# Kernel tuning notes

Hardware: AMD Instinct MI355X
Metric: run time of the kernel (lower is better)

Reference implementation:

```python
import jax, jax.numpy as jnp
import numpy as np
from jax import lax

# Static problem configuration (SAModule(ratio=0.25, r=0.2, MLP([35,64,64,128])))
B, N, C_IN = 8, 4096, 32
RATIO, R, K = 0.25, 0.2, 64   # K == max_num_neighbors
M = int(N * RATIO)            # centroids per cloud after FPS
NEG = -1e10


def setup_inputs() -> dict:
    key = jax.random.key(0)
    ks = jax.random.split(key, 6)
    x = jax.random.normal(ks[0], (B * N, C_IN), jnp.float32)
    pos = jax.random.uniform(ks[1], (B * N, 3), jnp.float32)  # unit cube -> r=0.2 balls are non-trivial
    batch = jnp.repeat(jnp.arange(B, dtype=jnp.int32), N)
    def lin(k, fan_in, fan_out):
        return jax.random.normal(k, (fan_in, fan_out), jnp.float32) * (1.0 / np.sqrt(fan_in))
    W1 = lin(ks[2], C_IN + 3, 64); b1 = jnp.zeros((64,), jnp.float32)
    W2 = lin(ks[3], 64, 64);       b2 = jnp.zeros((64,), jnp.float32)
    W3 = lin(ks[4], 64, 128);      b3 = jnp.zeros((128,), jnp.float32)
    return {"x": x, "pos": pos, "batch": batch,
            "W1": W1, "b1": b1, "W2": W2, "b2": b2, "W3": W3, "b3": b3}


def _fps_one(p):
    """Farthest-point sampling on one cloud p:[N,3] -> idx:[M] (deterministic start at 0)."""
    def body(carry, _):
        dmin, last = carry
        d = jnp.sum((p - p[last]) ** 2, axis=-1)         # [N] sq-dist to last picked point
        dmin = jnp.minimum(dmin, d)
        nxt = jnp.argmax(dmin).astype(jnp.int32)
        return (dmin, nxt), nxt
    init = (jnp.full((N,), 1e10, jnp.float32), jnp.int32(0))
    _, rest = lax.scan(body, init, None, length=M - 1)
    return jnp.concatenate([jnp.zeros((1,), jnp.int32), rest])


def _sa_one(p, xb, ib, W1, b1, W2, b2, W3, b3):
    """Radius ball-query + PointNetConv (gather -> MLP -> masked scatter-max) on one cloud."""
    ctr = p[ib]                                              # [M,3] sampled centroids
    d2 = jnp.sum((ctr[:, None, :] - p[None, :, :]) ** 2, -1)  # [M,N]
    negd, nbr = lax.top_k(-d2, K)                            # K nearest per centroid
    valid = (-negd) <= R * R                                 # inside-ball mask [M,K]
    xj = xb[nbr]                                             # [M,K,C_IN] gathered features
    rel = p[nbr] - ctr[:, None, :]                           # [M,K,3] relative positions
    h = jnp.concatenate([xj, rel], axis=-1)                  # message input [x_j, pos_j - pos_i]
    h = jax.nn.relu(h @ W1 + b1)
    h = jax.nn.relu(h @ W2 + b2)
    h = h @ W3 + b3                                          # plain last layer (PyG MLP plain_last)
    h = jnp.where(valid[..., None], h, NEG)
    return jnp.max(h, axis=1)                                # max aggregation -> [M,128]


def reference(x, pos, batch, W1, b1, W2, b2, W3, b3):
    pos3 = pos.reshape(B, N, 3)
    x3 = x.reshape(B, N, C_IN)
    idx = jax.vmap(_fps_one)(pos3)                           # [B,M]
    conv = lambda p, xb, ib: _sa_one(p, xb, ib, W1, b1, W2, b2, W3, b3)
    x_out = jax.vmap(conv)(pos3, x3, idx)                    # [B,M,128]
    pos_out = jnp.take_along_axis(pos3, idx[..., None], axis=1)  # [B,M,3]
    batch_out = jnp.repeat(jnp.arange(B, dtype=batch.dtype), M)
    return x_out.reshape(B * M, -1), pos_out.reshape(B * M, 3), batch_out
```

## Files before the change

### kernel.cpp

```cpp
#include <hip/hip_runtime.h>
#include <hip/hip_bf16.h>

#define BB 8
#define NN 4096
#define CIN 32
#define MM 1024
#define KNB 64
#define CAND 1024
#define FPS_T 256
#define FPS_PPT 16
#define ROWS 72

typedef __attribute__((ext_vector_type(8))) short  short8;
typedef __attribute__((ext_vector_type(4))) float  f32x4;

__device__ __forceinline__ float sq3(float dx, float dy, float dz) {
    return __fadd_rn(__fadd_rn(__fmul_rn(dx, dx), __fmul_rn(dy, dy)), __fmul_rn(dz, dz));
}

__device__ __forceinline__ unsigned short f2bf(float v) {
    union { __hip_bfloat16 b; unsigned short u; } cv;
    cv.b = __float2bfloat16(v);
    return cv.u;
}
__device__ __forceinline__ float bf2f(unsigned short u) {
    union { unsigned short u; __hip_bfloat16 b; } cv;
    cv.u = u;
    return __bfloat162float(cv.b);
}

static __device__ __forceinline__ f32x4 mfma16(short8 a, short8 b, f32x4 c) {
    return __builtin_amdgcn_mfma_f32_16x16x32_bf16(a, b, c, 0, 0, 0);
}

template<int CTRL>
__device__ __forceinline__ unsigned long long dpp_maxkey(unsigned long long k) {
    unsigned int lo = (unsigned int)k;
    unsigned int hi = (unsigned int)(k >> 32);
    unsigned int nlo = (unsigned int)__builtin_amdgcn_update_dpp((int)lo, (int)lo, CTRL, 0xF, 0xF, false);
    unsigned int nhi = (unsigned int)__builtin_amdgcn_update_dpp((int)hi, (int)hi, CTRL, 0xF, 0xF, false);
    unsigned long long nk = ((unsigned long long)nhi << 32) | (unsigned long long)nlo;
    return nk > k ? nk : k;
}

__global__ __launch_bounds__(256) void prep_kernel(
    const float* __restrict__ W1, const float* __restrict__ W2,
    const float* __restrict__ W3, unsigned short* __restrict__ wf)
{
    int gid = blockIdx.x * 256 + threadIdx.x;
    const float* W; int K, Ncol, base, slot;
    if (gid < 1024)      { W = W1; K = 35; Ncol = 64;  base = 0;     slot = gid; }
    else if (gid < 2048) { W = W2; K = 64; Ncol = 64;  base = 8192;  slot = gid - 1024; }
    else                 { W = W3; K = 64; Ncol = 128; base = 16384; slot = gid - 2048; }
    int lane = slot & 63, h = (slot >> 6) & 1, kstep = (slot >> 7) & 1, tile = slot >> 8;
    int col = tile * 16 + (lane & 15), quad = lane >> 4;
#pragma unroll
    for (int j = 0; j < 8; ++j) {
        int k = kstep * 32 + quad * 8 + j;
        float wv = (k < K) ? W[k * Ncol + col] : 0.0f;
        unsigned short hi = f2bf(wv);
        unsigned short v = h ? f2bf(wv - bf2f(hi)) : hi;
        wf[base + slot * 8 + j] = v;
    }
}

__global__ __launch_bounds__(FPS_T) void fps_kernel(
    const float* __restrict__ pos, int* __restrict__ idx_ws, float* __restrict__ out)
{
    const int b = blockIdx.x;
    const int t = threadIdx.x;
    __shared__ float4 plds4[NN];
    __shared__ int    chosen[MM];
    __shared__ __align__(16) unsigned long long part[2][FPS_T / 64];

    const float* P = pos + (size_t)b * NN * 3;
    for (int i = t; i < NN; i += FPS_T) {
        float4 v;
        v.x = P[3 * i]; v.y = P[3 * i + 1]; v.z = P[3 * i + 2]; v.w = 0.0f;
        plds4[i] = v;
    }
    if (t == 0) chosen[0] = 0;
    __syncthreads();

    float px[FPS_PPT], py[FPS_PPT], pz[FPS_PPT], dmin[FPS_PPT];
#pragma unroll
    for (int s = 0; s < FPS_PPT; ++s) {
        int i = t + FPS_T * s;
        float4 v = plds4[i];
        px[s] = v.x; py[s] = v.y; pz[s] = v.z;
        dmin[s] = 1e10f;
    }

    int win = 0;
    for (int it = 1; it < MM; ++it) {
        float4 wc = plds4[win];
        const float lx = wc.x, ly = wc.y, lz = wc.z;
        float bv = -1.0f;
        int   bi = 0;
#pragma unroll
        for (int s = 0; s < FPS_PPT; ++s) {
            float dx = px[s] - lx, dy = py[s] - ly, dz = pz[s] - lz;
            float d  = sq3(dx, dy, dz);
            float dm = fminf(dmin[s], d);
            dmin[s] = dm;
            if (dm > bv) { bv = dm; bi = t + FPS_T * s; }
        }
        unsigned long long k =
            ((unsigned long long)__float_as_uint(bv) << 32) | (unsigned int)(~bi);
        k = dpp_maxkey<0x111>(k);
        k = dpp_maxkey<0x112>(k);
        k = dpp_maxkey<0x114>(k);
        k = dpp_maxkey<0x118>(k);
        k = dpp_maxkey<0x142>(k);
        k = dpp_maxkey<0x143>(k);
        if ((t & 63) == 63) part[it & 1][t >> 6] = k;
        __syncthreads();
        const ulonglong2* pp = (const ulonglong2*)&part[it & 1][0];
        ulonglong2 p01 = pp[0], p23 = pp[1];
        unsigned long long ka = p01.x > p01.y ? p01.x : p01.y;
        unsigned long long kb = p23.x > p23.y ? p23.x : p23.y;
        unsigned long long km = ka > kb ? ka : kb;
        win = (int)(~(unsigned int)km);
        if (t == 0) chosen[it] = win;
    }
    __syncthreads();

    for (int m = t; m < MM; m += FPS_T) {
        int mi = chosen[m];
        idx_ws[b * MM + m] = mi;
        const int PO = BB * MM * 128;
        const int BO = PO + BB * MM * 3;
        int row = b * MM + m;
        float4 c = plds4[mi];
        out[PO + 3 * row + 0] = c.x;
        out[PO + 3 * row + 1] = c.y;
        out[PO + 3 * row + 2] = c.z;
        out[BO + row] = (float)b;
    }
}

__global__ __launch_bounds__(256, 4) void sa_kernel(
    const float* __restrict__ x, const float* __restrict__ pos,
    const int* __restrict__ idx_ws, const unsigned short* __restrict__ wf,
    const float* __restrict__ b1, const float* __restrict__ b2,
    const float* __restrict__ b3, float* __restrict__ out)
{
    const int bm = blockIdx.x;
    const int b  = bm >> 10;
    const int t  = threadIdx.x;
    const int w    = t >> 6;
    const int lane = t & 63;

    __shared__ unsigned short HA[2 * 64 * ROWS];
    __shared__ float cd2[CAND];
    __shared__ int   cid[CAND];
    __shared__ int   cnt;
    __shared__ int   sel[KNB];
    __shared__ float red[4][128];

    const float R2 = (float)(0.2 * 0.2);
    const float* P = pos + (size_t)b * NN * 3;
    const int ci = idx_ws[bm];

    if (t == 0) cnt = 0;
    __syncthreads();

    const float cx = P[3 * ci], cy = P[3 * ci + 1], cz = P[3 * ci + 2];

    for (int i = t; i < NN; i += 256) {
        float dx = P[3 * i] - cx, dy = P[3 * i + 1] - cy, dz = P[3 * i + 2] - cz;
        float d2 = sq3(dx, dy, dz);
        if (d2 <= R2) {
            int p = atomicAdd(&cnt, 1);
            if (p < CAND) { cd2[p] = d2; cid[p] = i; }
        }
    }
    __syncthreads();
    const int n = min(cnt, CAND);
    const int V = min(n, KNB);

    for (int i = t; i < n; i += 256) {
        float di = cd2[i];
        int   ii = cid[i];
        int rank = 0;
        for (int j = 0; j < n; ++j) {
            float dj = cd2[j];
            int   ij = cid[j];
            rank += (dj < di || (dj == di && ij < ii)) ? 1 : 0;
        }
        if (rank < KNB) sel[rank] = ii;
    }
    __syncthreads();

    {
        const int row = 16 * w + (lane & 15);
        const int prt = lane >> 4;
        short8 z = {};
        *(short8*)(HA + row * ROWS + 32 + prt * 8) = z;
        *(short8*)(HA + 64 * ROWS + row * ROWS + 32 + prt * 8) = z;
        if (row < V) {
            int g = b * NN + sel[row];
            const float4* xr = (const float4*)(x + (size_t)g * CIN + prt * 8);
            float4 v0 = xr[0], v1 = xr[1];
            float vv[8] = {v0.x, v0.y, v0.z, v0.w, v1.x, v1.y, v1.z, v1.w};
            short8 hv, lv;
#pragma unroll
            for (int j = 0; j < 8; ++j) {
                unsigned short h = f2bf(vv[j]);
                hv[j] = (short)h;
                lv[j] = (short)f2bf(vv[j] - bf2f(h));
            }
            *(short8*)(HA + row * ROWS + prt * 8) = hv;
            *(short8*)(HA + 64 * ROWS + row * ROWS + prt * 8) = lv;
            if (prt == 0) {
                int g2 = sel[row];
#pragma unroll
                for (int c = 0; c < 3; ++c) {
                    float cc = (c == 0) ? cx : (c == 1) ? cy : cz;
                    float rv = P[3 * g2 + c] - cc;
                    unsigned short h = f2bf(rv);
                    HA[row * ROWS + 32 + c] = h;
                    HA[64 * ROWS + row * ROWS + 32 + c] = f2bf(rv - bf2f(h));
                }
            }
        }
    }

    const int m16  = lane & 15;
    const int quad = lane >> 4;
    const int arow = 16 * w + m16;
    const short8* wf8 = (const short8*)wf;

    {
        short8 aH[2], aL[2];
        aH[0] = *(const short8*)(HA + arow * ROWS + quad * 8);
        aH[1] = *(const short8*)(HA + arow * ROWS + 32 + quad * 8);
        aL[0] = *(const short8*)(HA + 64 * ROWS + arow * ROWS + quad * 8);
        aL[1] = *(const short8*)(HA + 64 * ROWS + arow * ROWS + 32 + quad * 8);
#pragma unroll
        for (int tile = 0; tile < 4; ++tile) {
            f32x4 acc = {};
#pragma unroll
            for (int ks = 0; ks < 2; ++ks) {
                short8 bH = wf8[((tile * 2 + ks) * 2 + 0) * 64 + lane];
                short8 bL = wf8[((tile * 2 + ks) * 2 + 1) * 64 + lane];
                acc = mfma16(aH[ks], bH, acc);
                acc = mfma16(aH[ks], bL, acc);
                acc = mfma16(aL[ks], bH, acc);
            }
            int col = tile * 16 + m16;
            float bb = b1[col];
#pragma unroll
            for (int i = 0; i < 4; ++i) {
                int grow = 16 * w + quad * 4 + i;
                float v = fmaxf(acc[i] + bb, 0.0f);
                unsigned short h = f2bf(v);
                HA[grow * ROWS + col] = h;
                HA[64 * ROWS + grow * ROWS + col] = f2bf(v - bf2f(h));
            }
        }
    }

    {
        short8 aH[2], aL[2];
        aH[0] = *(const short8*)(HA + arow * ROWS + quad * 8);
        aH[1] = *(const short8*)(HA + arow * ROWS + 32 + quad * 8);
        aL[0] = *(const short8*)(HA + 64 * ROWS + arow * ROWS + quad * 8);
        aL[1] = *(const short8*)(HA + 64 * ROWS + arow * ROWS + 32 + quad * 8);
#pragma unroll
        for (int tile = 0; tile < 4; ++tile) {
            f32x4 acc = {};
#pragma unroll
            for (int ks = 0; ks < 2; ++ks) {
                short8 bH = wf8[1024 + ((tile * 2 + ks) * 2 + 0) * 64 + lane];
                short8 bL = wf8[1024 + ((tile * 2 + ks) * 2 + 1) * 64 + lane];
                acc = mfma16(aH[ks], bH, acc);
                acc = mfma16(aH[ks], bL, acc);
                acc = mfma16(aL[ks], bH, acc);
            }
            int col = tile * 16 + m16;
            float bb = b2[col];
#pragma unroll
            for (int i = 0; i < 4; ++i) {
                int grow = 16 * w + quad * 4 + i;
                float v = fmaxf(acc[i] + bb, 0.0f);
                unsigned short h = f2bf(v);
                HA[grow * ROWS + col] = h;
                HA[64 * ROWS + grow * ROWS + col] = f2bf(v - bf2f(h));
            }
        }
    }

    {
        short8 aH[2], aL[2];
        aH[0] = *(const short8*)(HA + arow * ROWS + quad * 8);
        aH[1] = *(const short8*)(HA + arow * ROWS + 32 + quad * 8);
        aL[0] = *(const short8*)(HA + 64 * ROWS + arow * ROWS + quad * 8);
        aL[1] = *(const short8*)(HA + 64 * ROWS + arow * ROWS + 32 + quad * 8);
#pragma unroll
        for (int tile = 0; tile < 8; ++tile) {
            f32x4 acc = {};
#pragma unroll
            for (int ks = 0; ks < 2; ++ks) {
                short8 bH = wf8[2048 + ((tile * 2 + ks) * 2 + 0) * 64 + lane];
                short8 bL = wf8[2048 + ((tile * 2 + ks) * 2 + 1) * 64 + lane];
                acc = mfma16(aH[ks], bH, acc);
                acc = mfma16(aH[ks], bL, acc);
                acc = mfma16(aL[ks], bH, acc);
            }
            float mv = -1e10f;
#pragma unroll
            for (int i = 0; i < 4; ++i) {
                int grow = 16 * w + quad * 4 + i;
                float v = (grow < V) ? acc[i] : -1e10f;
                mv = fmaxf(mv, v);
            }
            mv = fmaxf(mv, __shfl_xor(mv, 16));
            mv = fmaxf(mv, __shfl_xor(mv, 32));
            if (lane < 16) red[w][tile * 16 + lane] = mv;
        }
    }
    __syncthreads();

    if (t < 128) {
        float v = fmaxf(fmaxf(red[0][t], red[1][t]), fmaxf(red[2][t], red[3][t]));
        out[(size_t)bm * 128 + t] = v + b3[t];
    }
}

extern "C" void kernel_launch(void* const* d_in, const int* in_sizes, int n_in,
                              void* d_out, int out_size, void* d_ws, size_t ws_size,
                              hipStream_t stream) {
    const float* x   = (const float*)d_in[0];
    const float* pos = (const float*)d_in[1];
    const float* W1 = (const float*)d_in[3];
    const float* b1 = (const float*)d_in[4];
    const float* W2 = (const float*)d_in[5];
    const float* b2 = (const float*)d_in[6];
    const float* W3 = (const float*)d_in[7];
    const float* b3 = (const float*)d_in[8];
    float* out    = (float*)d_out;
    int*   idx_ws = (int*)d_ws;
    unsigned short* wf = (unsigned short*)((char*)d_ws + 32768);

    hipLaunchKernelGGL(prep_kernel, dim3(16), dim3(256), 0, stream, W1, W2, W3, wf);
    hipLaunchKernelGGL(fps_kernel, dim3(BB), dim3(FPS_T), 0, stream, pos, idx_ws, out);
    hipLaunchKernelGGL(sa_kernel, dim3(BB * MM), dim3(256), 0, stream,
                       x, pos, idx_ws, wf, b1, b2, b3, out);
}
```

Measured before the change: 799.7 us.

## Pack FPS math into float2 vectors and use packed-key ballot candidate ranking

The FPS inner loop now works on float2 vector pairs, which lets the compiler emit packed FP32 ops (v_pk_*), with contraction disabled so rounding stays the same. In the SA kernel, the per-thread atomic compaction is replaced by one atomic per wavefront, using a ballot and a popcount prefix. Candidates are now stored as packed 64-bit keys (distance bits, then index), so the O(n^2) rank loop does one 64-bit compare per pair instead of separate float and int loads and a tie-break. This relies on nonnegative float bit patterns ordering the same way as the floats, and it changes the order of points within each wavefront.

```diff
diff --git a/kernel.cpp b/kernel.cpp
--- a/kernel.cpp
+++ b/kernel.cpp
@@ -13,6 +13,7 @@
 
 typedef __attribute__((ext_vector_type(8))) short  short8;
 typedef __attribute__((ext_vector_type(4))) float  f32x4;
+typedef __attribute__((ext_vector_type(2))) float  f32x2;
 
 __device__ __forceinline__ float sq3(float dx, float dy, float dz) {
     return __fadd_rn(__fadd_rn(__fmul_rn(dx, dx), __fmul_rn(dy, dy)), __fmul_rn(dz, dz));
@@ -82,28 +83,41 @@
     if (t == 0) chosen[0] = 0;
     __syncthreads();
 
-    float px[FPS_PPT], py[FPS_PPT], pz[FPS_PPT], dmin[FPS_PPT];
-#pragma unroll
-    for (int s = 0; s < FPS_PPT; ++s) {
-        int i = t + FPS_T * s;
-        float4 v = plds4[i];
-        px[s] = v.x; py[s] = v.y; pz[s] = v.z;
-        dmin[s] = 1e10f;
+    f32x2 pxv[8], pyv[8], pzv[8], dminv[8];
+#pragma unroll
+    for (int s = 0; s < 8; ++s) {
+        float4 a = plds4[t + 512 * s];
+        float4 c = plds4[t + 512 * s + 256];
+        pxv[s] = (f32x2){a.x, c.x};
+        pyv[s] = (f32x2){a.y, c.y};
+        pzv[s] = (f32x2){a.z, c.z};
+        dminv[s] = (f32x2){1e10f, 1e10f};
     }
 
     int win = 0;
     for (int it = 1; it < MM; ++it) {
         float4 wc = plds4[win];
-        const float lx = wc.x, ly = wc.y, lz = wc.z;
+        const f32x2 lxv = (f32x2){wc.x, wc.x};
+        const f32x2 lyv = (f32x2){wc.y, wc.y};
+        const f32x2 lzv = (f32x2){wc.z, wc.z};
         float bv = -1.0f;
         int   bi = 0;
 #pragma unroll
-        for (int s = 0; s < FPS_PPT; ++s) {
-            float dx = px[s] - lx, dy = py[s] - ly, dz = pz[s] - lz;
-            float d  = sq3(dx, dy, dz);
-            float dm = fminf(dmin[s], d);
-            dmin[s] = dm;
-            if (dm > bv) { bv = dm; bi = t + FPS_T * s; }
+        for (int s = 0; s < 8; ++s) {
+            f32x2 d;
+            {
+#pragma clang fp contract(off)
+                f32x2 dx = pxv[s] - lxv;
+                f32x2 dy = pyv[s] - lyv;
+                f32x2 dz = pzv[s] - lzv;
+                d = dx * dx + dy * dy + dz * dz;
+            }
+            float m0 = fminf(dminv[s].x, d.x);
+            float m1 = fminf(dminv[s].y, d.y);
+            dminv[s].x = m0;
+            dminv[s].y = m1;
+            if (m0 > bv) { bv = m0; bi = t + 512 * s; }
+            if (m1 > bv) { bv = m1; bi = t + 512 * s + 256; }
         }
         unsigned long long k =
             ((unsigned long long)__float_as_uint(bv) << 32) | (unsigned int)(~bi);
@@ -152,8 +166,7 @@
     const int lane = t & 63;
 
     __shared__ unsigned short HA[2 * 64 * ROWS];
-    __shared__ float cd2[CAND];
-    __shared__ int   cid[CAND];
+    __shared__ unsigned long long candk[CAND];
     __shared__ int   cnt;
     __shared__ int   sel[KNB];
     __shared__ float red[4][128];
@@ -170,9 +183,19 @@
     for (int i = t; i < NN; i += 256) {
         float dx = P[3 * i] - cx, dy = P[3 * i + 1] - cy, dz = P[3 * i + 2] - cz;
         float d2 = sq3(dx, dy, dz);
-        if (d2 <= R2) {
-            int p = atomicAdd(&cnt, 1);
-            if (p < CAND) { cd2[p] = d2; cid[p] = i; }
+        bool hit = d2 <= R2;
+        unsigned long long m = __ballot(hit);
+        if (m) {
+            int leader = __ffsll((unsigned long long)m) - 1;
+            int base = 0;
+            if (lane == leader) base = atomicAdd(&cnt, __popcll(m));
+            base = __shfl(base, leader);
+            if (hit) {
+                int p = base + __popcll(m & ((1ull << lane) - 1));
+                if (p < CAND)
+                    candk[p] = ((unsigned long long)__float_as_uint(d2) << 32)
+                             | (unsigned int)i;
+            }
         }
     }
     __syncthreads();
@@ -180,15 +203,11 @@
     const int V = min(n, KNB);
 
     for (int i = t; i < n; i += 256) {
-        float di = cd2[i];
-        int   ii = cid[i];
+        unsigned long long ki = candk[i];
         int rank = 0;
-        for (int j = 0; j < n; ++j) {
-            float dj = cd2[j];
-            int   ij = cid[j];
-            rank += (dj < di || (dj == di && ij < ii)) ? 1 : 0;
-        }
-        if (rank < KNB) sel[rank] = ii;
+        for (int j = 0; j < n; ++j)
+            rank += (candk[j] < ki) ? 1 : 0;
+        if (rank < KNB) sel[rank] = (int)(ki & 0xffffffffu);
     }
     __syncthreads();
 
```

After: 793.6 us. Within noise of the previous version (-0.8%).
